# Performance work log

Hardware: AMD Instinct MI355X
Metric: run time of the kernel (lower is better)

Reference implementation:

```python
import jax, jax.numpy as jnp
import numpy as np

N_LAYERS = 8
DILATIONS = [1, 2, 1, 2, 1, 2, 1, 2]
K_HOPS = 3
BN = 13248   # batch(64) * n_nodes(207), merged as in the torch module
L = 13       # 12 history steps + 1; shrinks by sum(dilations)=12 across layers
E = 211968   # BN * avg_degree(16)


def _conv1d(x, w, b, dil):
    # x: (BN, Cin, L), w: (Cout, Cin, 2) kernel-2 dilated conv, VALID (causal shrink)
    y = jax.lax.conv_general_dilated(x, w, (1,), 'VALID', rhs_dilation=(dil,),
                                     dimension_numbers=('NCH', 'OIH', 'NCH'))
    return y + b[None, :, None]


def setup_inputs() -> dict:
    key = jax.random.key(0)
    ks = jax.random.split(key, 20)
    s = 0.1  # keep activations in a sane range
    return {
        'x': jax.random.normal(ks[0], (BN, L, 2), jnp.float32),
        'edge_src': jax.random.randint(ks[1], (E,), 0, BN),
        'edge_dst': jax.random.randint(ks[2], (E,), 0, BN),
        'edge_w': jax.random.uniform(ks[3], (E,), jnp.float32),
        'init_w': s * jax.random.normal(ks[4], (2, 32), jnp.float32),
        'init_b': s * jax.random.normal(ks[5], (32,), jnp.float32),
        'filt_w': s * jax.random.normal(ks[6], (8, 32, 32, 2), jnp.float32),
        'filt_b': s * jax.random.normal(ks[7], (8, 32), jnp.float32),
        'gate_w': s * jax.random.normal(ks[8], (8, 32, 32, 2), jnp.float32),
        'gate_b': s * jax.random.normal(ks[9], (8, 32), jnp.float32),
        'gcn_w': s * jax.random.normal(ks[10], (8, 6, 32, 32), jnp.float32),
        'gcn_b': s * jax.random.normal(ks[11], (8, 32), jnp.float32),
        'skip_w': s * jax.random.normal(ks[12], (8, 256, 32), jnp.float32),
        'skip_b': s * jax.random.normal(ks[13], (8, 256), jnp.float32),
        'out0_w': s * jax.random.normal(ks[14], (256, 512), jnp.float32),
        'out0_b': s * jax.random.normal(ks[15], (512,), jnp.float32),
        'out1_w': s * jax.random.normal(ks[16], (512, 12), jnp.float32),
        'out1_b': s * jax.random.normal(ks[17], (12,), jnp.float32),
    }


def reference(x, edge_src, edge_dst, edge_w, init_w, init_b,
              filt_w, filt_b, gate_w, gate_b, gcn_w, gcn_b,
              skip_w, skip_b, out0_w, out0_b, out1_w, out1_b):
    # init linear: (BN, L, 2) -> (BN, L, 32) -> (BN, 32, L)
    h = (x @ init_w + init_b).transpose(0, 2, 1)
    # per-hop edge weights: elementwise powers of the transition weights
    # (faithful to repo's dense_to_sparse(transition ** k)); bck = transposed edges
    adjs = [(edge_src, edge_dst, edge_w ** k) for k in range(1, K_HOPS + 1)] + \
           [(edge_dst, edge_src, edge_w ** k) for k in range(1, K_HOPS + 1)]
    skip = None
    for l in range(N_LAYERS):
        d = DILATIONS[l]
        res = h
        # Gated TCN: tanh(filter) * sigmoid(gate), seq shrinks by d
        t = jnp.tanh(_conv1d(h, filt_w[l], filt_b[l], d)) * \
            jax.nn.sigmoid(_conv1d(h, gate_w[l], gate_b[l], d))
        # Diffusion conv: sum over 6 adjacency types of A_w (x W_a)
        xt = t.transpose(0, 2, 1)  # (BN, L', 32)
        g = jnp.zeros_like(xt)
        for a, (src, dst, w) in enumerate(adjs):
            msg = (xt @ gcn_w[l, a])[src] * w[:, None, None]  # (E, L', 32)
            g = g + jax.ops.segment_sum(msg, dst, num_segments=BN)
        h = g.transpose(0, 2, 1) + gcn_b[l][None, :, None]  # (BN, 32, L')
        # residual connection (align shrunk sequence)
        h = h + res[:, :, -h.shape[-1]:]
        # skip conv (1x1) on last timestep, accumulated
        sc = h[:, :, -1] @ skip_w[l].T + skip_b[l]  # (BN, 256)
        skip = sc if skip is None else skip + sc
    out = jax.nn.relu(skip)
    out = jax.nn.relu(out @ out0_w + out0_b)
    return out @ out1_w + out1_b  # (BN, 12)
```

## Files before the change

### kernel.cpp

```cpp
#include <hip/hip_runtime.h>
#include <hip/hip_fp16.h>

#define BN 13248
#define NE 211968
#define NBKT 8
#define SCAN_TOT (BN * NBKT)
#define SCAN_NBLK 52
#define ZSTRIDE 200
#define HSTRIDE 40
#define HNODE 480

typedef __attribute__((ext_vector_type(8))) short bf16x8;
typedef __attribute__((ext_vector_type(8))) _Float16 f16x8;
typedef __attribute__((ext_vector_type(4))) float f32x4;

__device__ __forceinline__ f32x4 mfma16b(bf16x8 a, bf16x8 b, f32x4 c) {
  return __builtin_amdgcn_mfma_f32_16x16x32_bf16(a, b, c, 0, 0, 0);
}
__device__ __forceinline__ f32x4 mfma16h(f16x8 a, f16x8 b, f32x4 c) {
  return __builtin_amdgcn_mfma_f32_16x16x32_f16(a, b, c, 0, 0, 0);
}

__device__ __forceinline__ unsigned short to_bf16(float v) {
  unsigned bits = __float_as_uint(v);
  return (unsigned short)((bits + 0x7FFFu + ((bits >> 16) & 1u)) >> 16);
}
__device__ __forceinline__ unsigned short to_f16(float v) {
  union { __half h; unsigned short s; } u; u.h = __float2half(v); return u.s;
}
__device__ __forceinline__ unsigned h2u(__half2 h) {
  union { __half2 h; unsigned u; } v; v.h = h; return v.u;
}
__device__ __forceinline__ __half2 u2h(unsigned u) {
  union { unsigned u; __half2 h; } v; v.u = u; return v.h;
}

__device__ __forceinline__ float fast_tanh(float x) {
  float e2 = __expf(2.f * x);
  return 1.f - 2.f / (e2 + 1.f);
}
__device__ __forceinline__ float fast_sig(float x) {
  return 1.f / (1.f + __expf(-x));
}

__global__ void k_count(const int* __restrict__ src, const int* __restrict__ dst,
                        int* __restrict__ cur_f, int* __restrict__ cur_b) {
  int e = blockIdx.x * 256 + threadIdx.x;
  if (e < NE) {
    int s = src[e], t = dst[e];
    atomicAdd(&cur_f[t * NBKT + (s >> 11)], 1);
    atomicAdd(&cur_b[s * NBKT + (t >> 11)], 1);
  }
}

__global__ __launch_bounds__(1024) void k_scan1(int* __restrict__ cnt_f, int* __restrict__ cnt_b,
                                                int* __restrict__ bsum) {
  __shared__ int sdata[1024];
  int b = blockIdx.x;
  int dir = (b >= SCAN_NBLK) ? 1 : 0;
  int lb = dir ? b - SCAN_NBLK : b;
  int* cnt = dir ? cnt_b : cnt_f;
  int tid = threadIdx.x;
  int i0 = lb * 2048 + tid * 2;
  int v0 = (i0 < SCAN_TOT) ? cnt[i0] : 0;
  int v1 = (i0 + 1 < SCAN_TOT) ? cnt[i0 + 1] : 0;
  int tot = v0 + v1;
  sdata[tid] = tot;
  __syncthreads();
  for (int off = 1; off < 1024; off <<= 1) {
    int add = (tid >= off) ? sdata[tid - off] : 0;
    __syncthreads();
    sdata[tid] += add;
    __syncthreads();
  }
  int excl = sdata[tid] - tot;
  if (i0 < SCAN_TOT) cnt[i0] = excl;
  if (i0 + 1 < SCAN_TOT) cnt[i0 + 1] = excl + v0;
  if (tid == 1023) bsum[b] = sdata[1023];
}

__global__ void k_scan2(int* __restrict__ bsum) {
  __shared__ int sdata[128];
  int tid = threadIdx.x;
  int seg = (tid >= 64) ? 64 : 0;
  int src = (tid < 64) ? tid : tid - 64 + SCAN_NBLK;
  int valid = ((tid & 63) < SCAN_NBLK);
  int v = valid ? bsum[src] : 0;
  sdata[tid] = v;
  __syncthreads();
  for (int off = 1; off < 64; off <<= 1) {
    int add = (tid - off >= seg) ? sdata[tid - off] : 0;
    __syncthreads();
    sdata[tid] += add;
    __syncthreads();
  }
  if (valid) bsum[src] = sdata[tid] - v;
}

__global__ __launch_bounds__(1024) void k_scan3(int* __restrict__ cnt_f, int* __restrict__ cnt_b,
                                                const int* __restrict__ bsum,
                                                int* __restrict__ row_f, int* __restrict__ row_b) {
  int b = blockIdx.x;
  int dir = (b >= SCAN_NBLK) ? 1 : 0;
  int lb = dir ? b - SCAN_NBLK : b;
  int* cnt = dir ? cnt_b : cnt_f;
  int* row = dir ? row_b : row_f;
  int off = bsum[b];
  int tid = threadIdx.x;
#pragma unroll
  for (int k = 0; k < 2; ++k) {
    int idx = lb * 2048 + tid * 2 + k;
    if (idx < SCAN_TOT) {
      int v = cnt[idx] + off;
      cnt[idx] = v;
      if ((idx & (NBKT - 1)) == 0) row[idx / NBKT] = v;
    }
  }
  if (b == 0 && tid == 0) { row_f[BN] = NE; row_b[BN] = NE; }
}

__global__ void k_fill(const int* __restrict__ src, const int* __restrict__ dst,
                       const float* __restrict__ w,
                       int* __restrict__ cur_f, int4* __restrict__ ce_f,
                       int* __restrict__ cur_b, int4* __restrict__ ce_b) {
  int e = blockIdx.x * 256 + threadIdx.x;
  if (e < NE) {
    int s = src[e], t = dst[e];
    float wv = w[e];
    float w2 = wv * wv, w3 = w2 * wv;
    int u1 = (int)h2u(__float2half2_rn(wv));
    int u2 = (int)h2u(__float2half2_rn(w2));
    int u3 = (int)h2u(__float2half2_rn(w3));
    int p = atomicAdd(&cur_f[t * NBKT + (s >> 11)], 1); ce_f[p] = make_int4(s, u1, u2, u3);
    int q = atomicAdd(&cur_b[s * NBKT + (t >> 11)], 1); ce_b[q] = make_int4(t, u1, u2, u3);
  }
}

__global__ void k_init(const float* __restrict__ x, const float* __restrict__ iw,
                       const float* __restrict__ ib, float* __restrict__ h) {
  int idx = blockIdx.x * 256 + threadIdx.x;
  if (idx >= BN * 13 * 32) return;
  int c = idx & 31;
  int r = idx >> 5;
  int n = r % BN;
  int tau = r / BN;
  float x0 = x[(n * 13 + tau) * 2 + 0];
  float x1 = x[(n * 13 + tau) * 2 + 1];
  h[idx] = fmaf(x0, iw[c], fmaf(x1, iw[32 + c], ib[c]));
}

__global__ void k_pack(const float* __restrict__ skip_w, const float* __restrict__ skip_b,
                       const float* __restrict__ w0, const float* __restrict__ w1,
                       const float* __restrict__ gcn_w,
                       const float* __restrict__ filt_w, const float* __restrict__ gate_w,
                       unsigned short* __restrict__ SWb, unsigned short* __restrict__ W0T,
                       unsigned short* __restrict__ W1T, float* __restrict__ bsum,
                       unsigned short* __restrict__ Gg16, unsigned short* __restrict__ WTC) {
  int id = blockIdx.x * 256 + threadIdx.x;
  if (id < 65536) {
    int j = id >> 8, k = id & 255;
    SWb[id] = to_bf16(skip_w[((k >> 5) * 256 + j) * 32 + (k & 31)]);
  }
  if (id < 131072) {
    int jo = id >> 8, k = id & 255;
    W0T[id] = to_bf16(w0[k * 512 + jo]);
  }
  if (id < 8192) {
    int n = id >> 9, k = id & 511;
    W1T[id] = (n < 12) ? to_bf16(w1[k * 12 + n]) : (unsigned short)0;
  }
  if (id < 256) {
    float s = 0.f;
    for (int l = 0; l < 8; ++l) s += skip_b[l * 256 + id];
    bsum[id] = s;
  }
  if (id < 49152) {
    int l = id / 6144, rem = id % 6144;
    int co = rem / 192, k = rem % 192;
    int a = k >> 5, ci = k & 31;
    Gg16[id] = to_f16(gcn_w[((l * 6 + a) * 32 + ci) * 32 + co]);
  }
  if (id < 32768) {
    int l = id >> 12, rem = id & 4095;
    int g = rem >> 11, co = (rem >> 6) & 31, k = rem & 63;
    const float* srcw = (g ? gate_w : filt_w) + l * 2048;
    float v = (k < 32) ? srcw[(co * 32 + k) * 2 + 0] : srcw[(co * 32 + (k - 32)) * 2 + 1];
    WTC[id] = to_f16(v);
  }
}

template<int LIN, int D, int TPAD>
__global__ __launch_bounds__(256) void k_tcn(const float* __restrict__ h_in, unsigned short* __restrict__ t_out,
    const float* __restrict__ fw, const float* __restrict__ fb,
    const float* __restrict__ gw, const float* __restrict__ gb) {
  constexpr int LOUT = LIN - D;
  __shared__ __align__(16) float wq[32 * 32 * 4];
  __shared__ float hl[8][LIN * 32];
  int tid = threadIdx.x;
  for (int f = tid; f < 4096; f += 256) {
    int e = f & 3, co = (f >> 2) & 31, ci = f >> 7;
    const float* srcw = (e < 2) ? fw : gw;
    wq[f] = srcw[(co * 32 + ci) * 2 + (e & 1)];
  }
  int n0 = blockIdx.x * 8;
  for (int i = tid; i < 8 * LIN * 32; i += 256) {
    int c = i & 31, r = i >> 5;
    int nl = r / LIN, tau = r % LIN;
    hl[nl][tau * 32 + c] = h_in[(tau * BN + n0 + nl) * 32 + c];
  }
  __syncthreads();
  int nl = tid >> 5, co = tid & 31;
  int n = n0 + nl;
  float accf[LOUT], accg[LOUT];
  float fbv = fb[co], gbv = gb[co];
#pragma unroll
  for (int j = 0; j < LOUT; ++j) { accf[j] = fbv; accg[j] = gbv; }
#pragma unroll
  for (int ci = 0; ci < 32; ++ci) {
    float4 wv = *(const float4*)&wq[(ci * 32 + co) * 4];
    float xr[LIN];
#pragma unroll
    for (int t = 0; t < LIN; ++t) xr[t] = hl[nl][t * 32 + ci];
#pragma unroll
    for (int j = 0; j < LOUT; ++j) {
      accf[j] = fmaf(xr[j], wv.x, accf[j]);
      accf[j] = fmaf(xr[j + D], wv.y, accf[j]);
      accg[j] = fmaf(xr[j], wv.z, accg[j]);
      accg[j] = fmaf(xr[j + D], wv.w, accg[j]);
    }
  }
#pragma unroll
  for (int j = 0; j < TPAD; ++j) {
    unsigned short v = 0;
    if (j < LOUT) v = to_f16(fast_tanh(accf[j < LOUT ? j : 0]) * fast_sig(accg[j < LOUT ? j : 0]));
    t_out[(n * TPAD + j) * 32 + co] = v;
  }
}

template<int TPAD, int NT>
__device__ __forceinline__ void edge_fma(const int4& c, const uint2 (&u)[NT], __half2* A) {
  __half2 wh0 = u2h((unsigned)c.y), wh1 = u2h((unsigned)c.z), wh2 = u2h((unsigned)c.w);
#pragma unroll
  for (int j = 0; j < NT; ++j) {
    __half2 v0 = u2h(u[j].x), v1 = u2h(u[j].y);
    A[(0 * NT + j) * 2 + 0] = __hfma2(wh0, v0, A[(0 * NT + j) * 2 + 0]);
    A[(0 * NT + j) * 2 + 1] = __hfma2(wh0, v1, A[(0 * NT + j) * 2 + 1]);
    A[(1 * NT + j) * 2 + 0] = __hfma2(wh1, v0, A[(1 * NT + j) * 2 + 0]);
    A[(1 * NT + j) * 2 + 1] = __hfma2(wh1, v1, A[(1 * NT + j) * 2 + 1]);
    A[(2 * NT + j) * 2 + 0] = __hfma2(wh2, v0, A[(2 * NT + j) * 2 + 0]);
    A[(2 * NT + j) * 2 + 1] = __hfma2(wh2, v1, A[(2 * NT + j) * 2 + 1]);
  }
}

template<int TPAD, int NT, int LOUTT>
__device__ __forceinline__ void gather_dir(const unsigned short* __restrict__ t_in,
    int e0, int e1, const int4* __restrict__ ce, int rowoff0, int rowbase, __half2* A) {
  constexpr bool FULL = (LOUTT >= TPAD);
  constexpr int EB = 4;
  int e = e0;
  for (; e + EB <= e1; e += EB) {
    int4 c[EB];
    uint2 u[EB][NT];
#pragma unroll
    for (int k = 0; k < EB; ++k) c[k] = ce[e + k];
#pragma unroll
    for (int k = 0; k < EB; ++k) {
      const unsigned short* p = t_in + c[k].x * (TPAD * 32) + rowoff0;
#pragma unroll
      for (int j = 0; j < NT; ++j) {
        if (FULL || rowbase + j < LOUTT) u[k][j] = *(const uint2*)(p + j * 32);
        else u[k][j] = make_uint2(0u, 0u);
      }
    }
#pragma unroll
    for (int k = 0; k < EB; ++k) edge_fma<TPAD, NT>(c[k], u[k], A);
  }
  for (; e < e1; ++e) {
    int4 c = ce[e];
    uint2 u[NT];
    const unsigned short* p = t_in + c.x * (TPAD * 32) + rowoff0;
#pragma unroll
    for (int j = 0; j < NT; ++j) {
      if (FULL || rowbase + j < LOUTT) u[j] = *(const uint2*)(p + j * 32);
      else u[j] = make_uint2(0u, 0u);
    }
    edge_fma<TPAD, NT>(c, u, A);
  }
}

template<int LOUT, int D, int TPAD, int D2, int TPAD2, bool LAST>
__global__ __launch_bounds__(128, 4) void k_fused(
    const unsigned short* __restrict__ t_in,
    const float* __restrict__ h_in, float* __restrict__ h_out,
    float* __restrict__ lastcol, unsigned short* __restrict__ t_next,
    const int* __restrict__ row_f, const int4* __restrict__ ce_f,
    const int* __restrict__ row_b, const int4* __restrict__ ce_b,
    const unsigned short* __restrict__ Wg,
    const float* __restrict__ bias,
    const unsigned short* __restrict__ Wtc,
    const float* __restrict__ fbn, const float* __restrict__ gbn) {
  constexpr int NT = TPAD / 4;
  constexpr int LOUT2 = LAST ? 1 : (LOUT - D2);
  constexpr int SBYTES = 4 * TPAD * ZSTRIDE * 2;
  __shared__ __align__(16) char smem[SBYTES];
  unsigned short* Zl = (unsigned short*)smem;
  unsigned short* hb16 = (unsigned short*)smem;
  int tid = threadIdx.x;
  int nl = tid >> 5, lane32 = tid & 31;
  int tl = lane32 >> 3;
  int c4 = (lane32 & 7) << 2;
  int n0 = blockIdx.x * 4;
  int n = n0 + nl;
  int rowbase = tl * NT;
  int rowoff0 = rowbase * 32 + c4;
  int ef0 = row_f[n], ef1 = row_f[n + 1];
  int eb0 = row_b[n], eb1 = row_b[n + 1];
  __half2 acc[6 * NT * 2];
  __half2 zero = __float2half2_rn(0.f);
#pragma unroll
  for (int i = 0; i < 6 * NT * 2; ++i) acc[i] = zero;
  gather_dir<TPAD, NT, LOUT>(t_in, ef0, ef1, ce_f, rowoff0, rowbase, acc);
  gather_dir<TPAD, NT, LOUT>(t_in, eb0, eb1, ce_b, rowoff0, rowbase, acc + 3 * NT * 2);
#pragma unroll
  for (int j = 0; j < NT; ++j) {
    int m = nl * TPAD + rowbase + j;
#pragma unroll
    for (int a = 0; a < 6; ++a) {
      uint2 v = make_uint2(h2u(acc[(a * NT + j) * 2 + 0]), h2u(acc[(a * NT + j) * 2 + 1]));
      *(uint2*)(&Zl[m * ZSTRIDE + a * 32 + c4]) = v;
    }
  }
  __syncthreads();
  int wave = tid >> 6, lane = tid & 63;
  int m16 = lane & 15, q = lane >> 4;
  f32x4 dacc[NT];
#pragma unroll
  for (int i = 0; i < NT; ++i) {
    int u = wave * NT + i;
    int mt = u >> 1, nt = u & 1;
    dacc[i] = (f32x4){0.f, 0.f, 0.f, 0.f};
#pragma unroll
    for (int ks = 0; ks < 6; ++ks) {
      f16x8 av = *(const f16x8*)(&Zl[(mt * 16 + m16) * ZSTRIDE + ks * 32 + q * 8]);
      f16x8 bv = *(const f16x8*)((const _Float16*)Wg + (nt * 16 + m16) * 192 + ks * 32 + q * 8);
      dacc[i] = mfma16h(av, bv, dacc[i]);
    }
  }
  __syncthreads();
#pragma unroll
  for (int i = 0; i < NT; ++i) {
    int u = wave * NT + i;
    int mt = u >> 1, nt = u & 1;
    int co = nt * 16 + m16;
    float bco = bias[co];
#pragma unroll
    for (int r = 0; r < 4; ++r) {
      int mm = mt * 16 + q * 4 + r;
      int node = mm / TPAD;
      int tau = mm % TPAD;
      if (tau < LOUT) {
        float rres = h_in[((tau + D) * BN + n0 + node) * 32 + co];
        float o = dacc[i][r] + bco + rres;
        h_out[(tau * BN + n0 + node) * 32 + co] = o;
        if (!LAST) hb16[node * HNODE + tau * HSTRIDE + co] = to_f16(o);
        if (tau == LOUT - 1) lastcol[(n0 + node) * 32 + co] = o;
      }
    }
  }
  if (!LAST) {
    __syncthreads();
#pragma unroll
    for (int i = 0; i < 4; ++i) {
      int u = wave * 4 + i;
      int node = u >> 1, ntc = u & 1;
      int co = ntc * 16 + m16;
      f32x4 df = (f32x4){0.f, 0.f, 0.f, 0.f};
      f32x4 dg = (f32x4){0.f, 0.f, 0.f, 0.f};
#pragma unroll
      for (int s = 0; s < 2; ++s) {
        f16x8 av = *(const f16x8*)(&hb16[node * HNODE + (m16 + s * D2) * HSTRIDE + q * 8]);
        f16x8 bvf = *(const f16x8*)((const _Float16*)Wtc + (0 * 32 + co) * 64 + s * 32 + q * 8);
        f16x8 bvg = *(const f16x8*)((const _Float16*)Wtc + (1 * 32 + co) * 64 + s * 32 + q * 8);
        df = mfma16h(av, bvf, df);
        dg = mfma16h(av, bvg, dg);
      }
      float fbv = fbn[co], gbv = gbn[co];
#pragma unroll
      for (int r = 0; r < 4; ++r) {
        int j = q * 4 + r;
        if (j < TPAD2) {
          unsigned short v = 0;
          if (j < LOUT2)
            v = to_f16(fast_tanh(df[r] + fbv) * fast_sig(dg[r] + gbv));
          t_next[((n0 + node) * TPAD2 + j) * 32 + co] = v;
        }
      }
    }
  }
}

__device__ __forceinline__ bf16x8 ldsA(const unsigned short* buf, int stride, int row, int ks, int q) {
  int unit = ks * 4 + q;
  int addr = row * stride + ((unit ^ (row & 7)) << 3);
  return *(const bf16x8*)(buf + addr);
}

__global__ __launch_bounds__(256) void k_final(const float* __restrict__ lastcol,
    const unsigned short* __restrict__ SWb, const unsigned short* __restrict__ W0T,
    const unsigned short* __restrict__ W1T, const float* __restrict__ bsum,
    const float* __restrict__ b0, const float* __restrict__ b1,
    float* __restrict__ out) {
  __shared__ __align__(16) unsigned short Z[32 * 256];
  __shared__ __align__(16) unsigned short H[32 * 512];
  int tid = threadIdx.x;
  int wave = tid >> 6, lane = tid & 63;
  int m16 = lane & 15, q = lane >> 4;
  int n0 = blockIdx.x * 32;
#pragma unroll
  for (int it = 0; it < 32; ++it) {
    int id = it * 256 + tid;
    int m = id >> 8, k = id & 255;
    float v = lastcol[((k >> 5) * BN + n0 + m) * 32 + (k & 31)];
    Z[m * 256 + (((k >> 3) ^ (m & 7)) << 3) + (k & 7)] = to_bf16(v);
  }
  __syncthreads();
  f32x4 acc1[2][4];
#pragma unroll
  for (int mt = 0; mt < 2; ++mt)
#pragma unroll
    for (int i = 0; i < 4; ++i) acc1[mt][i] = (f32x4){0.f, 0.f, 0.f, 0.f};
#pragma unroll
  for (int ks = 0; ks < 8; ++ks) {
    bf16x8 a0 = ldsA(Z, 256, m16, ks, q);
    bf16x8 a1 = ldsA(Z, 256, 16 + m16, ks, q);
#pragma unroll
    for (int i = 0; i < 4; ++i) {
      int j = (wave * 4 + i) * 16 + m16;
      bf16x8 b = *(const bf16x8*)(SWb + j * 256 + ks * 32 + q * 8);
      acc1[0][i] = mfma16b(a0, b, acc1[0][i]);
      acc1[1][i] = mfma16b(a1, b, acc1[1][i]);
    }
  }
  __syncthreads();
#pragma unroll
  for (int i = 0; i < 4; ++i) {
    int j = (wave * 4 + i) * 16 + m16;
    float bs = bsum[j];
#pragma unroll
    for (int mt = 0; mt < 2; ++mt)
#pragma unroll
      for (int r = 0; r < 4; ++r) {
        int row = mt * 16 + q * 4 + r;
        float v = fmaxf(acc1[mt][i][r] + bs, 0.f);
        Z[row * 256 + (((j >> 3) ^ (row & 7)) << 3) + (j & 7)] = to_bf16(v);
      }
  }
  __syncthreads();
  f32x4 acc2[2][8];
#pragma unroll
  for (int mt = 0; mt < 2; ++mt)
#pragma unroll
    for (int i = 0; i < 8; ++i) acc2[mt][i] = (f32x4){0.f, 0.f, 0.f, 0.f};
#pragma unroll
  for (int ks = 0; ks < 8; ++ks) {
    bf16x8 a0 = ldsA(Z, 256, m16, ks, q);
    bf16x8 a1 = ldsA(Z, 256, 16 + m16, ks, q);
#pragma unroll
    for (int i = 0; i < 8; ++i) {
      int jo = (wave * 8 + i) * 16 + m16;
      bf16x8 b = *(const bf16x8*)(W0T + jo * 256 + ks * 32 + q * 8);
      acc2[0][i] = mfma16b(a0, b, acc2[0][i]);
      acc2[1][i] = mfma16b(a1, b, acc2[1][i]);
    }
  }
#pragma unroll
  for (int i = 0; i < 8; ++i) {
    int jo = (wave * 8 + i) * 16 + m16;
    float b0v = b0[jo];
#pragma unroll
    for (int mt = 0; mt < 2; ++mt)
#pragma unroll
      for (int r = 0; r < 4; ++r) {
        int row = mt * 16 + q * 4 + r;
        float v = fmaxf(acc2[mt][i][r] + b0v, 0.f);
        H[row * 512 + (((jo >> 3) ^ (row & 7)) << 3) + (jo & 7)] = to_bf16(v);
      }
  }
  __syncthreads();
  if (wave < 2) {
    f32x4 acc3 = (f32x4){0.f, 0.f, 0.f, 0.f};
#pragma unroll
    for (int ks = 0; ks < 16; ++ks) {
      bf16x8 a = ldsA(H, 512, wave * 16 + m16, ks, q);
      bf16x8 b = *(const bf16x8*)(W1T + m16 * 512 + ks * 32 + q * 8);
      acc3 = mfma16b(a, b, acc3);
    }
    if (m16 < 12) {
      float bv = b1[m16];
#pragma unroll
      for (int r = 0; r < 4; ++r)
        out[(n0 + wave * 16 + q * 4 + r) * 12 + m16] = acc3[r] + bv;
    }
  }
}

extern "C" void kernel_launch(void* const* d_in, const int* in_sizes, int n_in,
                              void* d_out, int out_size, void* d_ws, size_t ws_size,
                              hipStream_t stream) {
  const float* x      = (const float*)d_in[0];
  const int*   esrc   = (const int*)d_in[1];
  const int*   edst   = (const int*)d_in[2];
  const float* ew     = (const float*)d_in[3];
  const float* init_w = (const float*)d_in[4];
  const float* init_b = (const float*)d_in[5];
  const float* filt_w = (const float*)d_in[6];
  const float* filt_b = (const float*)d_in[7];
  const float* gate_w = (const float*)d_in[8];
  const float* gate_b = (const float*)d_in[9];
  const float* gcn_w  = (const float*)d_in[10];
  const float* gcn_b  = (const float*)d_in[11];
  const float* skip_w = (const float*)d_in[12];
  const float* skip_b = (const float*)d_in[13];
  const float* w0     = (const float*)d_in[14];
  const float* b0     = (const float*)d_in[15];
  const float* w1     = (const float*)d_in[16];
  const float* b1     = (const float*)d_in[17];
  float* out = (float*)d_out;

  float* base = (float*)d_ws;
  float* hA      = base;
  float* hB      = hA + 13 * BN * 32;
  unsigned short* tA = (unsigned short*)(hB + 13 * BN * 32);
  unsigned short* tB = tA + 12 * BN * 32;
  float* lastcol = (float*)(tB + 12 * BN * 32);
  int* row_f = (int*)(lastcol + 8 * BN * 32);
  int* row_b = row_f + (BN + 2);
  int* bscan = row_b + (BN + 2);
  int* cur_f = bscan + 128;
  int* cur_b = cur_f + BN * NBKT;
  int4* ce_f = (int4*)(cur_b + BN * NBKT);
  int4* ce_b = ce_f + NE;
  unsigned short* SWb  = (unsigned short*)(ce_b + NE);
  unsigned short* W0T  = SWb + 65536;
  unsigned short* W1T  = W0T + 131072;
  unsigned short* Gg16 = W1T + 8192;
  unsigned short* WTC  = Gg16 + 49152;
  float* bsumv = (float*)(WTC + 32768);

  hipMemsetAsync(cur_f, 0, 2 * BN * NBKT * sizeof(int), stream);
  const int egrid = (NE + 255) / 256;
  k_count<<<egrid, 256, 0, stream>>>(esrc, edst, cur_f, cur_b);
  k_scan1<<<2 * SCAN_NBLK, 1024, 0, stream>>>(cur_f, cur_b, bscan);
  k_scan2<<<1, 128, 0, stream>>>(bscan);
  k_scan3<<<2 * SCAN_NBLK, 1024, 0, stream>>>(cur_f, cur_b, bscan, row_f, row_b);
  k_fill<<<egrid, 256, 0, stream>>>(esrc, edst, ew, cur_f, ce_f, cur_b, ce_b);
  k_init<<<(BN * 13 * 32 + 255) / 256, 256, 0, stream>>>(x, init_w, init_b, hA);
  k_pack<<<512, 256, 0, stream>>>(skip_w, skip_b, w0, w1, gcn_w, filt_w, gate_w,
                                  SWb, W0T, W1T, bsumv, Gg16, WTC);

  k_tcn<13, 1, 12><<<BN / 8, 256, 0, stream>>>(hA, tA, filt_w, filt_b, gate_w, gate_b);

#define FUSED(l, LOUTv, Dv, TPv, D2v, TP2v, LASTv, tin, tout, hin, hout) \
  k_fused<LOUTv, Dv, TPv, D2v, TP2v, LASTv><<<BN / 4, 128, 0, stream>>>( \
      tin, hin, hout, lastcol + l * BN * 32, tout, row_f, ce_f, row_b, ce_b, \
      Gg16 + l * 6144, gcn_b + l * 32, WTC + (l + 1) * 4096, \
      filt_b + (l + 1) * 32, gate_b + (l + 1) * 32);

  FUSED(0, 12, 1, 12, 2, 12, false, tA, tB, hA, hB)
  FUSED(1, 10, 2, 12, 1, 12, false, tB, tA, hB, hA)
  FUSED(2,  9, 1, 12, 2,  8, false, tA, tB, hA, hB)
  FUSED(3,  7, 2,  8, 1,  8, false, tB, tA, hB, hA)
  FUSED(4,  6, 1,  8, 2,  4, false, tA, tB, hA, hB)
  FUSED(5,  4, 2,  4, 1,  4, false, tB, tA, hB, hA)
  FUSED(6,  3, 1,  4, 2,  4, false, tA, tB, hA, hB)
#undef FUSED
  k_fused<1, 2, 4, 2, 4, true><<<BN / 4, 128, 0, stream>>>(
      tB, hB, hA, lastcol + 7 * BN * 32, tA, row_f, ce_f, row_b, ce_b,
      Gg16 + 7 * 6144, gcn_b + 7 * 32, WTC, filt_b, gate_b);

  k_final<<<BN / 32, 256, 0, stream>>>(lastcol, SWb, W0T, W1T, bsumv, b0, b1, out);
}
```

Measured before the change: 621.3 us.

## Split forward/backward edge gathers across half-waves, two nodes per block

Each fused layer block now handles two nodes instead of four. The two 32-lane halves of each wave gather the forward and backward edge lists in parallel rather than one after the other, which halves per-thread accumulator registers and the serial gather length. The gather loop also prefetches the next batch of edge descriptors, fences scheduling with a sched_barrier, and uses a batch of 8 edges when NT==1. The trade-off is twice as many blocks, padded MMA rows for small TPAD, and a smaller per-wave MFMA share, which may waste some tensor work.

```diff
diff --git a/kernel.cpp b/kernel.cpp
--- a/kernel.cpp
+++ b/kernel.cpp
@@ -237,8 +237,8 @@
   }
 }
 
-template<int TPAD, int NT>
-__device__ __forceinline__ void edge_fma(const int4& c, const uint2 (&u)[NT], __half2* A) {
+template<int NT>
+__device__ __forceinline__ void edge_fma3(const int4& c, const uint2 (&u)[NT], __half2* A) {
   __half2 wh0 = u2h((unsigned)c.y), wh1 = u2h((unsigned)c.z), wh2 = u2h((unsigned)c.w);
 #pragma unroll
   for (int j = 0; j < NT; ++j) {
@@ -253,38 +253,48 @@
 }
 
 template<int TPAD, int NT, int LOUTT>
-__device__ __forceinline__ void gather_dir(const unsigned short* __restrict__ t_in,
+__device__ __forceinline__ void gather_one(const unsigned short* __restrict__ t_in,
     int e0, int e1, const int4* __restrict__ ce, int rowoff0, int rowbase, __half2* A) {
   constexpr bool FULL = (LOUTT >= TPAD);
-  constexpr int EB = 4;
+  constexpr int EB = (NT == 1) ? 8 : 4;
   int e = e0;
-  for (; e + EB <= e1; e += EB) {
-    int4 c[EB];
+  int4 c[EB];
+  if (e + EB <= e1) {
+#pragma unroll
+    for (int k = 0; k < EB; ++k) c[k] = ce[e + k];
+  }
+  while (e + EB <= e1) {
     uint2 u[EB][NT];
-#pragma unroll
-    for (int k = 0; k < EB; ++k) c[k] = ce[e + k];
 #pragma unroll
     for (int k = 0; k < EB; ++k) {
       const unsigned short* p = t_in + c[k].x * (TPAD * 32) + rowoff0;
 #pragma unroll
-      for (int j = 0; j < NT; ++j) {
-        if (FULL || rowbase + j < LOUTT) u[k][j] = *(const uint2*)(p + j * 32);
-        else u[k][j] = make_uint2(0u, 0u);
-      }
-    }
-#pragma unroll
-    for (int k = 0; k < EB; ++k) edge_fma<TPAD, NT>(c[k], u[k], A);
+      for (int j = 0; j < NT; ++j)
+        u[k][j] = (FULL || rowbase + j < LOUTT) ? *(const uint2*)(p + j * 32) : make_uint2(0u, 0u);
+    }
+    e += EB;
+    int4 cn[EB];
+    bool more = (e + EB <= e1);
+    if (more) {
+#pragma unroll
+      for (int k = 0; k < EB; ++k) cn[k] = ce[e + k];
+    }
+    __builtin_amdgcn_sched_barrier(0);
+#pragma unroll
+    for (int k = 0; k < EB; ++k) edge_fma3<NT>(c[k], u[k], A);
+    if (more) {
+#pragma unroll
+      for (int k = 0; k < EB; ++k) c[k] = cn[k];
+    }
   }
   for (; e < e1; ++e) {
-    int4 c = ce[e];
-    uint2 u[NT];
-    const unsigned short* p = t_in + c.x * (TPAD * 32) + rowoff0;
-#pragma unroll
-    for (int j = 0; j < NT; ++j) {
-      if (FULL || rowbase + j < LOUTT) u[j] = *(const uint2*)(p + j * 32);
-      else u[j] = make_uint2(0u, 0u);
-    }
-    edge_fma<TPAD, NT>(c, u, A);
+    int4 c1 = ce[e];
+    uint2 u1[NT];
+    const unsigned short* p = t_in + c1.x * (TPAD * 32) + rowoff0;
+#pragma unroll
+    for (int j = 0; j < NT; ++j)
+      u1[j] = (FULL || rowbase + j < LOUTT) ? *(const uint2*)(p + j * 32) : make_uint2(0u, 0u);
+    edge_fma3<NT>(c1, u1, A);
   }
 }
 
@@ -301,42 +311,47 @@
     const float* __restrict__ fbn, const float* __restrict__ gbn) {
   constexpr int NT = TPAD / 4;
   constexpr int LOUT2 = LAST ? 1 : (LOUT - D2);
-  constexpr int SBYTES = 4 * TPAD * ZSTRIDE * 2;
+  constexpr int ZROWS = (2 * TPAD + 15) & ~15;
+  constexpr int SBYTES = ZROWS * ZSTRIDE * 2;
   __shared__ __align__(16) char smem[SBYTES];
   unsigned short* Zl = (unsigned short*)smem;
   unsigned short* hb16 = (unsigned short*)smem;
   int tid = threadIdx.x;
-  int nl = tid >> 5, lane32 = tid & 31;
+  int nl = tid >> 6;
+  int lane = tid & 63;
+  int dh = lane >> 5;
+  int lane32 = lane & 31;
   int tl = lane32 >> 3;
   int c4 = (lane32 & 7) << 2;
-  int n0 = blockIdx.x * 4;
+  int n0 = blockIdx.x * 2;
   int n = n0 + nl;
   int rowbase = tl * NT;
   int rowoff0 = rowbase * 32 + c4;
-  int ef0 = row_f[n], ef1 = row_f[n + 1];
-  int eb0 = row_b[n], eb1 = row_b[n + 1];
-  __half2 acc[6 * NT * 2];
+  const int* rowp = dh ? row_b : row_f;
+  const int4* ce  = dh ? ce_b : ce_f;
+  int e0 = rowp[n], e1 = rowp[n + 1];
+  __half2 acc[3 * NT * 2];
   __half2 zero = __float2half2_rn(0.f);
 #pragma unroll
-  for (int i = 0; i < 6 * NT * 2; ++i) acc[i] = zero;
-  gather_dir<TPAD, NT, LOUT>(t_in, ef0, ef1, ce_f, rowoff0, rowbase, acc);
-  gather_dir<TPAD, NT, LOUT>(t_in, eb0, eb1, ce_b, rowoff0, rowbase, acc + 3 * NT * 2);
+  for (int i = 0; i < 3 * NT * 2; ++i) acc[i] = zero;
+  gather_one<TPAD, NT, LOUT>(t_in, e0, e1, ce, rowoff0, rowbase, acc);
 #pragma unroll
   for (int j = 0; j < NT; ++j) {
     int m = nl * TPAD + rowbase + j;
 #pragma unroll
-    for (int a = 0; a < 6; ++a) {
-      uint2 v = make_uint2(h2u(acc[(a * NT + j) * 2 + 0]), h2u(acc[(a * NT + j) * 2 + 1]));
-      *(uint2*)(&Zl[m * ZSTRIDE + a * 32 + c4]) = v;
-    }
-  }
-  __syncthreads();
-  int wave = tid >> 6, lane = tid & 63;
+    for (int a3 = 0; a3 < 3; ++a3) {
+      uint2 v = make_uint2(h2u(acc[(a3 * NT + j) * 2 + 0]), h2u(acc[(a3 * NT + j) * 2 + 1]));
+      *(uint2*)(&Zl[m * ZSTRIDE + (dh * 3 + a3) * 32 + c4]) = v;
+    }
+  }
+  __syncthreads();
+  int wave = nl;
   int m16 = lane & 15, q = lane >> 4;
-  f32x4 dacc[NT];
-#pragma unroll
-  for (int i = 0; i < NT; ++i) {
-    int u = wave * NT + i;
+  constexpr int UPW = ZROWS / 16;
+  f32x4 dacc[UPW];
+#pragma unroll
+  for (int i = 0; i < UPW; ++i) {
+    int u = wave * UPW + i;
     int mt = u >> 1, nt = u & 1;
     dacc[i] = (f32x4){0.f, 0.f, 0.f, 0.f};
 #pragma unroll
@@ -348,8 +363,8 @@
   }
   __syncthreads();
 #pragma unroll
-  for (int i = 0; i < NT; ++i) {
-    int u = wave * NT + i;
+  for (int i = 0; i < UPW; ++i) {
+    int u = wave * UPW + i;
     int mt = u >> 1, nt = u & 1;
     int co = nt * 16 + m16;
     float bco = bias[co];
@@ -358,7 +373,7 @@
       int mm = mt * 16 + q * 4 + r;
       int node = mm / TPAD;
       int tau = mm % TPAD;
-      if (tau < LOUT) {
+      if (mm < 2 * TPAD && tau < LOUT) {
         float rres = h_in[((tau + D) * BN + n0 + node) * 32 + co];
         float o = dacc[i][r] + bco + rres;
         h_out[(tau * BN + n0 + node) * 32 + co] = o;
@@ -370,8 +385,8 @@
   if (!LAST) {
     __syncthreads();
 #pragma unroll
-    for (int i = 0; i < 4; ++i) {
-      int u = wave * 4 + i;
+    for (int i = 0; i < 2; ++i) {
+      int u = wave * 2 + i;
       int node = u >> 1, ntc = u & 1;
       int co = ntc * 16 + m16;
       f32x4 df = (f32x4){0.f, 0.f, 0.f, 0.f};
@@ -561,7 +576,7 @@
   k_tcn<13, 1, 12><<<BN / 8, 256, 0, stream>>>(hA, tA, filt_w, filt_b, gate_w, gate_b);
 
 #define FUSED(l, LOUTv, Dv, TPv, D2v, TP2v, LASTv, tin, tout, hin, hout) \
-  k_fused<LOUTv, Dv, TPv, D2v, TP2v, LASTv><<<BN / 4, 128, 0, stream>>>( \
+  k_fused<LOUTv, Dv, TPv, D2v, TP2v, LASTv><<<BN / 2, 128, 0, stream>>>( \
       tin, hin, hout, lastcol + l * BN * 32, tout, row_f, ce_f, row_b, ce_b, \
       Gg16 + l * 6144, gcn_b + l * 32, WTC + (l + 1) * 4096, \
       filt_b + (l + 1) * 32, gate_b + (l + 1) * 32);
@@ -574,7 +589,7 @@
   FUSED(5,  4, 2,  4, 1,  4, false, tB, tA, hB, hA)
   FUSED(6,  3, 1,  4, 2,  4, false, tA, tB, hA, hB)
 #undef FUSED
-  k_fused<1, 2, 4, 2, 4, true><<<BN / 4, 128, 0, stream>>>(
+  k_fused<1, 2, 4, 2, 4, true><<<BN / 2, 128, 0, stream>>>(
       tB, hB, hA, lastcol + 7 * BN * 32, tA, row_f, ce_f, row_b, ce_b,
       Gg16 + 7 * 6144, gcn_b + 7 * 32, WTC, filt_b, gate_b);
 
```

Measured after the change: 831.4 us. +33.8%, slower.
